# Kernel optimization log

Measured on AMD Instinct MI355X. Metric: run time of the kernel, lower is better.

## Reference

```python
import jax, jax.numpy as jnp
import numpy as np

B, H, W, DIM, NH = 2, 48, 48, 768, 12
HD = DIM // NH  # 64


def setup_inputs() -> dict:
    key = jax.random.key(0)
    ks = jax.random.split(key, 7)
    std = 0.02
    return {
        "x": jax.random.normal(ks[0], (B, H, W, DIM), jnp.float32),
        "rel_pos_h": jax.random.normal(ks[1], (2 * H - 1, HD), jnp.float32) * std,
        "rel_pos_w": jax.random.normal(ks[2], (2 * W - 1, HD), jnp.float32) * std,
        "qkv_w": jax.random.normal(ks[3], (3 * DIM, DIM), jnp.float32) * std,
        "qkv_b": jnp.zeros((3 * DIM,), jnp.float32),
        "proj_w": jax.random.normal(ks[4], (DIM, DIM), jnp.float32) * std,
        "proj_b": jnp.zeros((DIM,), jnp.float32),
    }


def reference(x, rel_pos_h, rel_pos_w, qkv_w, qkv_b, proj_w, proj_b):
    b, h, w, dim = x.shape
    nh = NH
    hd = dim // nh
    scale = hd ** -0.5
    n = h * w
    # qkv projection: (B,N,3*dim) -> (3, B*nh, N, hd)
    qkv = x.reshape(b, n, dim) @ qkv_w.T + qkv_b
    qkv = qkv.reshape(b, n, 3, nh, hd).transpose(2, 0, 3, 1, 4).reshape(3, b * nh, n, hd)
    q, k, v = qkv[0], qkv[1], qkv[2]
    # scaled dot-product scores (B*nh, N, N)
    attn = jnp.einsum('bnc,bmc->bnm', q * scale, k)
    # decomposed relative position bias (q_size == k_size, no interpolation)
    idx_h = jnp.arange(h)[:, None] - jnp.arange(h)[None, :] + (h - 1)  # (h,h)
    idx_w = jnp.arange(w)[:, None] - jnp.arange(w)[None, :] + (w - 1)  # (w,w)
    Rh = rel_pos_h[idx_h]  # (h, h, hd)
    Rw = rel_pos_w[idx_w]  # (w, w, hd)
    r_q = q.reshape(b * nh, h, w, hd)
    rel_h = jnp.einsum('bhwc,hkc->bhwk', r_q, Rh)  # (B*nh, h, w, h)
    rel_w = jnp.einsum('bhwc,wkc->bhwk', r_q, Rw)  # (B*nh, h, w, w)
    attn = (attn.reshape(b * nh, h, w, h, w)
            + rel_h[:, :, :, :, None]
            + rel_w[:, :, :, None, :]).reshape(b * nh, n, n)
    attn = jax.nn.softmax(attn, axis=-1)
    out = (attn @ v).reshape(b, nh, h, w, hd).transpose(0, 2, 3, 1, 4).reshape(b, h, w, dim)
    return out @ proj_w.T + proj_b
```

## Files before the change

### kernel.cpp

```cpp
#include <hip/hip_runtime.h>
#include <hip/hip_bf16.h>
#include <stdint.h>

#define NQ    2304
#define MROWS 4608
#define DIMC  768
#define NHEAD 12
#define HEADS 24
#define HD    64

typedef unsigned int uint;
typedef unsigned short u16;
typedef __attribute__((ext_vector_type(8))) short s16x8;
typedef __attribute__((ext_vector_type(4))) float f32x4;

#define MFMA16(a, b, c) __builtin_amdgcn_mfma_f32_16x16x32_bf16((a), (b), (c), 0, 0, 0)

static __device__ __forceinline__ float bfbits2f(uint u) {
  union { uint i; float f; } c; c.i = u << 16; return c.f;
}
static __device__ __forceinline__ u16 f2bf(float f) {
  __hip_bfloat16 h = __float2bfloat16(f);
  union { __hip_bfloat16 h; u16 u; } c; c.h = h; return c.u;
}
static __device__ __forceinline__ u16 f2h(float f) {
  union { _Float16 h; u16 u; } c; c.h = (_Float16)f; return c.u;
}
static __device__ __forceinline__ float h2f(u16 u) {
  union { u16 u; _Float16 h; } c; c.u = u; return (float)c.h;
}
static __device__ __forceinline__ void dec8(uint4 p, float* f) {
  f[0] = bfbits2f(p.x & 0xFFFFu); f[1] = bfbits2f(p.x >> 16);
  f[2] = bfbits2f(p.y & 0xFFFFu); f[3] = bfbits2f(p.y >> 16);
  f[4] = bfbits2f(p.z & 0xFFFFu); f[5] = bfbits2f(p.z >> 16);
  f[6] = bfbits2f(p.w & 0xFFFFu); f[7] = bfbits2f(p.w >> 16);
}
static __device__ __forceinline__ void ld8(const void* p, size_t idx, int bf, float* f) {
  if (bf) { dec8(*(const uint4*)((const u16*)p + idx), f); }
  else {
    const float4* q = (const float4*)((const float*)p + idx);
    float4 a = q[0], b = q[1];
    f[0] = a.x; f[1] = a.y; f[2] = a.z; f[3] = a.w;
    f[4] = b.x; f[5] = b.y; f[6] = b.z; f[7] = b.w;
  }
}
static __device__ __forceinline__ float ld1(const void* p, size_t idx, int bf) {
  return bf ? bfbits2f(((const u16*)p)[idx]) : ((const float*)p)[idx];
}
static __device__ __forceinline__ uint4 ld8_to_bf(const void* p, size_t idx, int bf) {
  if (bf) return *(const uint4*)((const u16*)p + idx);
  float f[8]; ld8(p, idx, 0, f);
  uint4 u;
  u.x = (uint)f2bf(f[0]) | ((uint)f2bf(f[1]) << 16);
  u.y = (uint)f2bf(f[2]) | ((uint)f2bf(f[3]) << 16);
  u.z = (uint)f2bf(f[4]) | ((uint)f2bf(f[5]) << 16);
  u.w = (uint)f2bf(f[6]) | ((uint)f2bf(f[7]) << 16);
  return u;
}

__global__ __launch_bounds__(64) void detect_k(const u16* __restrict__ x,
                                               int* __restrict__ mode) {
  int t = threadIdx.x;
  int cnt = 0;
  for (int i = 0; i < 32; ++i) {
    uint u = x[(size_t)(t * 32 + i) * 2];
    uint e = (u >> 7) & 0xFFu;
    uint mag = u & 0x7FFFu;
    if (mag == 0 || (e >= 113 && e <= 133)) cnt++;
  }
#pragma unroll
  for (int d = 1; d < 64; d <<= 1) cnt += __shfl_xor(cnt, d);
  if (t == 0) mode[0] = (cnt > 1024) ? 1 : 0;
}

__global__ __launch_bounds__(256) void qkv_gemm_k(
    const void* __restrict__ Xp, const void* __restrict__ Wp,
    const void* __restrict__ Bq, const int* __restrict__ mode,
    u16* __restrict__ Q, u16* __restrict__ K, u16* __restrict__ Vt)
{
  __shared__ __align__(16) u16 As[128][40];
  __shared__ __align__(16) u16 Bs[128][40];
  const int bf = mode[0];
  const int t = threadIdx.x;
  const int w = t >> 6, l15 = t & 15, quad = (t >> 4) & 3;
  const int wr = w >> 1, wc = w & 1;
  const int row0 = blockIdx.y << 7, col0 = blockIdx.x << 7;
  const int lr = t >> 1, lk = (t & 1) << 4;

  f32x4 zero4 = {0.f, 0.f, 0.f, 0.f};
  f32x4 acc[4][4];
#pragma unroll
  for (int i = 0; i < 4; ++i)
#pragma unroll
    for (int j = 0; j < 4; ++j) acc[i][j] = zero4;

  for (int kt = 0; kt < DIMC; kt += 32) {
    __syncthreads();
    *(uint4*)&As[lr][lk]     = ld8_to_bf(Xp, (size_t)(row0 + lr) * DIMC + kt + lk, bf);
    *(uint4*)&As[lr][lk + 8] = ld8_to_bf(Xp, (size_t)(row0 + lr) * DIMC + kt + lk + 8, bf);
    *(uint4*)&Bs[lr][lk]     = ld8_to_bf(Wp, (size_t)(col0 + lr) * DIMC + kt + lk, bf);
    *(uint4*)&Bs[lr][lk + 8] = ld8_to_bf(Wp, (size_t)(col0 + lr) * DIMC + kt + lk + 8, bf);
    __syncthreads();
    s16x8 af[4], bfr[4];
#pragma unroll
    for (int i = 0; i < 4; ++i)
      af[i] = *(const s16x8*)&As[(wr << 6) + (i << 4) + l15][quad << 3];
#pragma unroll
    for (int j = 0; j < 4; ++j)
      bfr[j] = *(const s16x8*)&Bs[(wc << 6) + (j << 4) + l15][quad << 3];
#pragma unroll
    for (int i = 0; i < 4; ++i)
#pragma unroll
      for (int j = 0; j < 4; ++j)
        acc[i][j] = MFMA16(af[i], bfr[j], acc[i][j]);
  }

#pragma unroll
  for (int jt = 0; jt < 4; ++jt) {
    int col = col0 + (wc << 6) + (jt << 4) + l15;
    int which = col / DIMC;
    int rem = col - which * DIMC;
    int head = rem >> 6, d = rem & 63;
    float bv = ld1(Bq, col, bf);
#pragma unroll
    for (int i = 0; i < 4; ++i)
#pragma unroll
      for (int r = 0; r < 4; ++r) {
        int mrow = row0 + (wr << 6) + (i << 4) + (quad << 2) + r;
        int b_ = (mrow >= NQ) ? 1 : 0;
        int n = mrow - b_ * NQ;
        u16 val = f2bf(acc[i][jt][r] + bv);
        size_t bh = (size_t)(b_ * NHEAD + head);
        if (which == 2)      Vt[(bh * HD + d) * NQ + n] = val;
        else if (which == 1) K[(bh * NQ + n) * HD + d] = val;
        else                 Q[(bh * NQ + n) * HD + d] = val;
      }
  }
}

__global__ __launch_bounds__(256) void bias_gemm_k(
    const u16* __restrict__ Qw,
    const void* __restrict__ rph, const void* __restrict__ rpw,
    const int* __restrict__ mode,
    u16* __restrict__ Bh_g, u16* __restrict__ Bw_g)
{
  __shared__ __align__(16) u16 As[128][72];
  __shared__ __align__(16) u16 Bs[192][72];
  const int bf = mode[0];
  const int t = threadIdx.x;
  const int w = t >> 6, l15 = t & 15, quad = (t >> 4) & 3;
  const int wr = w >> 1, wc = w & 1;
  const int blk = blockIdx.x;
  const int bhd = blk / 18;
  const int row0 = (blk - bhd * 18) << 7;

  {
    int lr = t >> 1, lk = (t & 1) << 5;
    const u16* src = Qw + ((size_t)bhd * NQ + row0 + lr) * HD + lk;
    *(uint4*)&As[lr][lk]      = *(const uint4*)(src);
    *(uint4*)&As[lr][lk + 8]  = *(const uint4*)(src + 8);
    *(uint4*)&As[lr][lk + 16] = *(const uint4*)(src + 16);
    *(uint4*)&As[lr][lk + 24] = *(const uint4*)(src + 24);
  }
  for (int e = t; e < 384; e += 256) {
    int row = e >> 1, k32 = (e & 1) << 5;
    int tab = (row >= 96) ? 1 : 0;
    int r2 = row - (tab ? 96 : 0);
    if (r2 > 94) r2 = 0;
    const void* src = tab ? rpw : rph;
    *(uint4*)&Bs[row][k32]      = ld8_to_bf(src, (size_t)r2 * HD + k32, bf);
    *(uint4*)&Bs[row][k32 + 8]  = ld8_to_bf(src, (size_t)r2 * HD + k32 + 8, bf);
    *(uint4*)&Bs[row][k32 + 16] = ld8_to_bf(src, (size_t)r2 * HD + k32 + 16, bf);
    *(uint4*)&Bs[row][k32 + 24] = ld8_to_bf(src, (size_t)r2 * HD + k32 + 24, bf);
  }
  __syncthreads();

  f32x4 zero4 = {0.f, 0.f, 0.f, 0.f};
  f32x4 acc[4][6];
#pragma unroll
  for (int i = 0; i < 4; ++i)
#pragma unroll
    for (int j = 0; j < 6; ++j) acc[i][j] = zero4;

#pragma unroll
  for (int ks = 0; ks < 2; ++ks) {
    s16x8 af[4], bfr[6];
#pragma unroll
    for (int i = 0; i < 4; ++i)
      af[i] = *(const s16x8*)&As[(wr << 6) + (i << 4) + l15][(ks << 5) + (quad << 3)];
#pragma unroll
    for (int j = 0; j < 6; ++j)
      bfr[j] = *(const s16x8*)&Bs[wc * 96 + (j << 4) + l15][(ks << 5) + (quad << 3)];
#pragma unroll
    for (int i = 0; i < 4; ++i)
#pragma unroll
      for (int j = 0; j < 6; ++j)
        acc[i][j] = MFMA16(af[i], bfr[j], acc[i][j]);
  }

#pragma unroll
  for (int jt = 0; jt < 6; ++jt) {
    int col = wc * 96 + (jt << 4) + l15;
    int tab = (col >= 96) ? 1 : 0;
    int j = col - (tab ? 96 : 0);
    if (j >= 95) continue;
    u16* dstT = tab ? Bw_g : Bh_g;
#pragma unroll
    for (int i = 0; i < 4; ++i)
#pragma unroll
      for (int r = 0; r < 4; ++r) {
        int n = row0 + (wr << 6) + (i << 4) + (quad << 2) + r;
        int qh = (n * 10923) >> 19;
        int coord = tab ? (n - qh * 48) : qh;
        int c = coord + 47 - j;
        if (c >= 0 && c < 48)
          dstT[((size_t)bhd * 48 + c) * NQ + n] = f2h(acc[i][jt][r]);
      }
  }
}

__global__ __launch_bounds__(256) void attn_k(
    const u16* __restrict__ Qw, const u16* __restrict__ Kw,
    const u16* __restrict__ Vtg,
    const u16* __restrict__ Bh_g, const u16* __restrict__ Bw_g,
    int S, float* __restrict__ Opart, float* __restrict__ Lpart,
    u16* __restrict__ Aout)
{
  __shared__ __align__(16) u16 BhL[48][128];
  __shared__ __align__(16) u16 BwL[128][52];

  const int bid = blockIdx.x;
  const int xcd = bid & 7;
  const int local = bid >> 3;
  const int per_head = 18 * S;
  const int head_l = local / per_head;
  const int rem = local - head_l * per_head;
  const int qb = rem / S;
  const int z = rem - qb * S;
  const int bhd = xcd * 3 + head_l;
  const int q0 = qb << 7;
  const int span = NQ / S;
  const int kt_lo = z * span, kt_hi = kt_lo + span;

  const int t = threadIdx.x;
  const int w = t >> 6, l15 = t & 15, quad = (t >> 4) & 3;
  const float scale = 0.125f;

  const u16* kbase  = Kw  + (size_t)bhd * NQ * HD;
  const u16* vtbase = Vtg + (size_t)bhd * HD * NQ;
  const int q0w = q0 + (w << 5);

  for (int e = t; e < 48 * 128; e += 256) {
    int c = e >> 7, r = e & 127;
    size_t gi = ((size_t)bhd * 48 + c) * NQ + q0 + r;
    BhL[c][r] = Bh_g[gi];
    BwL[r][c] = Bw_g[gi];
  }

  s16x8 qa0[2], qa1[2];
#pragma unroll
  for (int g = 0; g < 2; ++g) {
    const u16* qfrag = Qw + ((size_t)bhd * NQ + q0w + (g << 4) + l15) * HD + (quad << 3);
    qa0[g] = *(const s16x8*)(qfrag);
    qa1[g] = *(const s16x8*)(qfrag + 32);
  }

  __syncthreads();

  f32x4 zero4 = {0.f, 0.f, 0.f, 0.f};
  f32x4 acc_o[2][4];
#pragma unroll
  for (int g = 0; g < 2; ++g)
#pragma unroll
    for (int nc = 0; nc < 4; ++nc) acc_o[g][nc] = zero4;
  float l_st[2] = {0.f, 0.f};
  const int srcA = ((quad & 1) << 5) + l15;
  const int srcB = srcA + 16;
  const int hi = quad >> 1;
  int km = 0;

  for (int kt0 = kt_lo; kt0 < kt_hi; kt0 += 64) {
    f32x4 acc_s[2][4];
#pragma unroll
    for (int nc = 0; nc < 4; ++nc) {
      const u16* kp = kbase + (size_t)(kt0 + (nc << 4) + l15) * HD + (quad << 3);
      s16x8 kb0 = *(const s16x8*)(kp);
      s16x8 kb1 = *(const s16x8*)(kp + 32);
      f32x4 a0 = MFMA16(kb0, qa0[0], zero4);
      acc_s[0][nc] = MFMA16(kb1, qa1[0], a0);
      f32x4 a1 = MFMA16(kb0, qa0[1], zero4);
      acc_s[1][nc] = MFMA16(kb1, qa1[1], a1);
    }

    int kh0 = (kt0 * 10923) >> 19;
    int thr = (kh0 + 1) * 48 - kt0;
    uint Wq[2][8];
#pragma unroll
    for (int g = 0; g < 2; ++g) {
      int qrl = (w << 5) + (g << 4) + l15;
      float bh0v = h2f(BhL[kh0][qrl]);
      float bh1v = h2f(BhL[kh0 + 1][qrl]);
      float sum = 0.f;
#pragma unroll
      for (int nc = 0; nc < 4; ++nc) {
        int bnc = km + (nc << 4);
        bnc = (bnc >= 48) ? bnc - 48 : bnc;
        uint2 pv = *(const uint2*)&BwL[qrl][bnc + (quad << 2)];
        float b0 = h2f((u16)(pv.x & 0xFFFFu));
        float b1 = h2f((u16)(pv.x >> 16));
        float b2 = h2f((u16)(pv.y & 0xFFFFu));
        float b3 = h2f((u16)(pv.y >> 16));
        int kl = (nc << 4) + (quad << 2);
        float e0 = __expf(acc_s[g][nc][0] * scale + ((kl     >= thr) ? bh1v : bh0v) + b0);
        float e1 = __expf(acc_s[g][nc][1] * scale + ((kl + 1 >= thr) ? bh1v : bh0v) + b1);
        float e2 = __expf(acc_s[g][nc][2] * scale + ((kl + 2 >= thr) ? bh1v : bh0v) + b2);
        float e3 = __expf(acc_s[g][nc][3] * scale + ((kl + 3 >= thr) ? bh1v : bh0v) + b3);
        sum += (e0 + e1) + (e2 + e3);
        Wq[g][2 * nc]     = (uint)f2bf(e0) | ((uint)f2bf(e1) << 16);
        Wq[g][2 * nc + 1] = (uint)f2bf(e2) | ((uint)f2bf(e3) << 16);
      }
      l_st[g] += sum;
    }

#pragma unroll
    for (int h = 0; h < 2; ++h) {
      s16x8 vb[4];
#pragma unroll
      for (int nc = 0; nc < 4; ++nc)
        vb[nc] = *(const s16x8*)(vtbase + (size_t)((nc << 4) + l15) * NQ
                                 + kt0 + (h << 5) + (quad << 3));
#pragma unroll
      for (int g = 0; g < 2; ++g) {
        uint e0 = __shfl(Wq[g][4*h+0], srcA), e1 = __shfl(Wq[g][4*h+1], srcA);
        uint e2 = __shfl(Wq[g][4*h+2], srcA), e3 = __shfl(Wq[g][4*h+3], srcA);
        uint g0 = __shfl(Wq[g][4*h+0], srcB), g1 = __shfl(Wq[g][4*h+1], srcB);
        uint g2 = __shfl(Wq[g][4*h+2], srcB), g3 = __shfl(Wq[g][4*h+3], srcB);
        union { uint u[4]; s16x8 v; } pf;
        pf.u[0] = hi ? e2 : e0; pf.u[1] = hi ? e3 : e1;
        pf.u[2] = hi ? g2 : g0; pf.u[3] = hi ? g3 : g1;
#pragma unroll
        for (int nc = 0; nc < 4; ++nc)
          acc_o[g][nc] = MFMA16(pf.v, vb[nc], acc_o[g][nc]);
      }
    }
    km += 16;
    if (km >= 48) km -= 48;
  }

#pragma unroll
  for (int g = 0; g < 2; ++g) {
    float lg = l_st[g];
    lg += __shfl_xor(lg, 16);
    lg += __shfl_xor(lg, 32);
    if (S > 1) {
      float* Op = Opart + ((size_t)(z * HEADS + bhd) * NQ + q0) * HD;
#pragma unroll
      for (int r = 0; r < 4; ++r) {
        int row = (w << 5) + (g << 4) + (quad << 2) + r;
#pragma unroll
        for (int nc = 0; nc < 4; ++nc)
          Op[(size_t)row * HD + (nc << 4) + l15] = acc_o[g][nc][r];
      }
      if (quad == 0)
        Lpart[(size_t)(z * HEADS + bhd) * NQ + q0w + (g << 4) + l15] = lg;
    } else {
      int b_ = bhd / NHEAD, head = bhd - b_ * NHEAD;
      float invl = 1.f / lg;
      int bsrc = (quad << 4) + (quad << 2);
#pragma unroll
      for (int r = 0; r < 4; ++r) {
        float inv = __shfl(invl, bsrc + r);
        int token = q0 + (w << 5) + (g << 4) + (quad << 2) + r;
        u16* dst = Aout + ((size_t)b_ * NQ + token) * DIMC + (head << 6);
#pragma unroll
        for (int nc = 0; nc < 4; ++nc)
          dst[(nc << 4) + l15] = f2bf(acc_o[g][nc][r] * inv);
      }
    }
  }
}

__global__ __launch_bounds__(256) void combine_k(
    const float* __restrict__ Op, const float* __restrict__ Lp,
    int S, u16* __restrict__ Aout)
{
  int idx = blockIdx.x * 256 + threadIdx.x;
  int m = idx / 192;
  int cq = idx - m * 192;
  int ccol = cq << 2;
  int head = ccol >> 6, d0 = ccol & 63;
  int b_ = (m >= NQ) ? 1 : 0;
  int n = m - b_ * NQ;
  int bh = b_ * NHEAD + head;
  float ox = 0.f, oy = 0.f, oz = 0.f, ow = 0.f, ls = 0.f;
  for (int zz = 0; zz < S; ++zz) {
    const float* ob = Op + ((size_t)(zz * HEADS + bh) * NQ + n) * HD + d0;
    float4 v = *(const float4*)ob;
    ox += v.x; oy += v.y; oz += v.z; ow += v.w;
    ls += Lp[(size_t)(zz * HEADS + bh) * NQ + n];
  }
  float inv = 1.f / ls;
  u16* dst = Aout + (size_t)m * DIMC + ccol;
  dst[0] = f2bf(ox * inv); dst[1] = f2bf(oy * inv);
  dst[2] = f2bf(oz * inv); dst[3] = f2bf(ow * inv);
}

__global__ __launch_bounds__(256) void proj_gemm_k(
    const u16* __restrict__ A, const void* __restrict__ Wp,
    const void* __restrict__ Bp, const int* __restrict__ mode,
    void* __restrict__ Out)
{
  __shared__ __align__(16) u16 As[128][40];
  __shared__ __align__(16) u16 Bs[128][40];
  const int bf = mode[0];
  const int t = threadIdx.x;
  const int w = t >> 6, l15 = t & 15, quad = (t >> 4) & 3;
  const int wr = w >> 1, wc = w & 1;
  const int row0 = blockIdx.y << 7, col0 = blockIdx.x << 7;
  const int lr = t >> 1, lk = (t & 1) << 4;

  f32x4 zero4 = {0.f, 0.f, 0.f, 0.f};
  f32x4 acc[4][4];
#pragma unroll
  for (int i = 0; i < 4; ++i)
#pragma unroll
    for (int j = 0; j < 4; ++j) acc[i][j] = zero4;

  for (int kt = 0; kt < DIMC; kt += 32) {
    __syncthreads();
    *(uint4*)&As[lr][lk]     = *(const uint4*)(A + (size_t)(row0 + lr) * DIMC + kt + lk);
    *(uint4*)&As[lr][lk + 8] = *(const uint4*)(A + (size_t)(row0 + lr) * DIMC + kt + lk + 8);
    *(uint4*)&Bs[lr][lk]     = ld8_to_bf(Wp, (size_t)(col0 + lr) * DIMC + kt + lk, bf);
    *(uint4*)&Bs[lr][lk + 8] = ld8_to_bf(Wp, (size_t)(col0 + lr) * DIMC + kt + lk + 8, bf);
    __syncthreads();
    s16x8 af[4], bfr[4];
#pragma unroll
    for (int i = 0; i < 4; ++i)
      af[i] = *(const s16x8*)&As[(wr << 6) + (i << 4) + l15][quad << 3];
#pragma unroll
    for (int j = 0; j < 4; ++j)
      bfr[j] = *(const s16x8*)&Bs[(wc << 6) + (j << 4) + l15][quad << 3];
#pragma unroll
    for (int i = 0; i < 4; ++i)
#pragma unroll
      for (int j = 0; j < 4; ++j)
        acc[i][j] = MFMA16(af[i], bfr[j], acc[i][j]);
  }

#pragma unroll
  for (int jt = 0; jt < 4; ++jt) {
    int col = col0 + (wc << 6) + (jt << 4) + l15;
    float bv = ld1(Bp, col, bf);
#pragma unroll
    for (int i = 0; i < 4; ++i)
#pragma unroll
      for (int r = 0; r < 4; ++r) {
        int mrow = row0 + (wr << 6) + (i << 4) + (quad << 2) + r;
        float val = acc[i][jt][r] + bv;
        size_t off = (size_t)mrow * DIMC + col;
        if (bf) ((u16*)Out)[off] = f2bf(val);
        else    ((float*)Out)[off] = val;
      }
  }
}

extern "C" void kernel_launch(void* const* d_in, const int* in_sizes, int n_in,
                              void* d_out, int out_size, void* d_ws, size_t ws_size,
                              hipStream_t stream)
{
  const void* x    = d_in[0];
  const void* rph  = d_in[1];
  const void* rpw  = d_in[2];
  const void* qkvw = d_in[3];
  const void* qkvb = d_in[4];
  const void* pw   = d_in[5];
  const void* pb   = d_in[6];

  int* mode = (int*)d_ws;
  const size_t qkv_elems = (size_t)HEADS * NQ * HD;
  u16* q    = (u16*)((char*)d_ws + 16);
  u16* k    = q + qkv_elems;
  u16* vt   = k + qkv_elems;
  u16* aout = vt + qkv_elems;
  const size_t base = 16 + 4 * qkv_elems * 2;
  const size_t biasElems = (size_t)HEADS * 48 * NQ;
  u16* bh_g = (u16*)((char*)d_ws + base);
  u16* bw_g = bh_g + biasElems;
  const size_t base2 = base + 2 * biasElems * 2;
  const size_t perO = (size_t)HEADS * NQ * HD * 4;
  const size_t perL = (size_t)HEADS * NQ * 4;

  int S = 1;
  if (ws_size >= base2 + 3 * (perO + perL)) S = 3;
  else if (ws_size >= base2 + 2 * (perO + perL)) S = 2;
  float* opart = (float*)((char*)d_ws + base2);
  float* lpart = (float*)((char*)d_ws + base2 + (size_t)S * perO);

  detect_k<<<1, 64, 0, stream>>>((const u16*)x, mode);
  qkv_gemm_k<<<dim3(18, 36), 256, 0, stream>>>(x, qkvw, qkvb, mode, q, k, vt);
  bias_gemm_k<<<dim3(432), 256, 0, stream>>>(q, rph, rpw, mode, bh_g, bw_g);
  attn_k<<<dim3(432 * S), 256, 0, stream>>>(q, k, vt, bh_g, bw_g,
                                            S, opart, lpart, aout);
  if (S > 1)
    combine_k<<<dim3(3456), 256, 0, stream>>>(opart, lpart, S, aout);
  proj_gemm_k<<<dim3(6, 36), 256, 0, stream>>>(aout, pw, pb, mode, d_out);
}
```

Baseline: 381.6 us.

## Double attention query tile to 256 rows and interleave QK/softmax/PV per half

Each attention block now covers 256 query rows (64 per wave) instead of 128, so every K and V tile loaded from global memory is reused across twice as many queries, and the grid is halved. The score MFMA, bias-add/exp and PV MFMA are restructured to work per 32-key half, which limits how many score registers are live at once. The bias tile staging into LDS now uses 16-byte vector loads. The cost is more accumulator registers per thread and fewer blocks, which can lower occupancy and leave CUs idle.

```diff
diff --git a/kernel.cpp b/kernel.cpp
--- a/kernel.cpp
+++ b/kernel.cpp
@@ -226,19 +226,19 @@
     int S, float* __restrict__ Opart, float* __restrict__ Lpart,
     u16* __restrict__ Aout)
 {
-  __shared__ __align__(16) u16 BhL[48][128];
-  __shared__ __align__(16) u16 BwL[128][52];
+  __shared__ __align__(16) u16 BhL[48][256];
+  __shared__ __align__(16) u16 BwL[256][52];
 
   const int bid = blockIdx.x;
   const int xcd = bid & 7;
   const int local = bid >> 3;
-  const int per_head = 18 * S;
+  const int per_head = 9 * S;
   const int head_l = local / per_head;
   const int rem = local - head_l * per_head;
   const int qb = rem / S;
   const int z = rem - qb * S;
   const int bhd = xcd * 3 + head_l;
-  const int q0 = qb << 7;
+  const int q0 = qb << 8;
   const int span = NQ / S;
   const int kt_lo = z * span, kt_hi = kt_lo + span;
 
@@ -248,18 +248,26 @@
 
   const u16* kbase  = Kw  + (size_t)bhd * NQ * HD;
   const u16* vtbase = Vtg + (size_t)bhd * HD * NQ;
-  const int q0w = q0 + (w << 5);
-
-  for (int e = t; e < 48 * 128; e += 256) {
-    int c = e >> 7, r = e & 127;
-    size_t gi = ((size_t)bhd * 48 + c) * NQ + q0 + r;
-    BhL[c][r] = Bh_g[gi];
-    BwL[r][c] = Bw_g[gi];
-  }
-
-  s16x8 qa0[2], qa1[2];
-#pragma unroll
-  for (int g = 0; g < 2; ++g) {
+  const int q0w = q0 + (w << 6);
+
+  for (int e = t; e < 1536; e += 256) {
+    int c = e >> 5;
+    int off = (e & 31) << 3;
+    size_t gi = ((size_t)bhd * 48 + c) * NQ + q0 + off;
+    *(uint4*)&BhL[c][off] = *(const uint4*)(Bh_g + gi);
+    uint4 wv = *(const uint4*)(Bw_g + gi);
+    u16 vals[8];
+    vals[0] = wv.x & 0xFFFFu; vals[1] = wv.x >> 16;
+    vals[2] = wv.y & 0xFFFFu; vals[3] = wv.y >> 16;
+    vals[4] = wv.z & 0xFFFFu; vals[5] = wv.z >> 16;
+    vals[6] = wv.w & 0xFFFFu; vals[7] = wv.w >> 16;
+#pragma unroll
+    for (int j = 0; j < 8; ++j) BwL[off + j][c] = vals[j];
+  }
+
+  s16x8 qa0[4], qa1[4];
+#pragma unroll
+  for (int g = 0; g < 4; ++g) {
     const u16* qfrag = Qw + ((size_t)bhd * NQ + q0w + (g << 4) + l15) * HD + (quad << 3);
     qa0[g] = *(const s16x8*)(qfrag);
     qa1[g] = *(const s16x8*)(qfrag + 32);
@@ -268,73 +276,65 @@
   __syncthreads();
 
   f32x4 zero4 = {0.f, 0.f, 0.f, 0.f};
-  f32x4 acc_o[2][4];
-#pragma unroll
-  for (int g = 0; g < 2; ++g)
+  f32x4 acc_o[4][4];
+#pragma unroll
+  for (int g = 0; g < 4; ++g)
 #pragma unroll
     for (int nc = 0; nc < 4; ++nc) acc_o[g][nc] = zero4;
-  float l_st[2] = {0.f, 0.f};
+  float l_st[4] = {0.f, 0.f, 0.f, 0.f};
   const int srcA = ((quad & 1) << 5) + l15;
   const int srcB = srcA + 16;
   const int hi = quad >> 1;
   int km = 0;
 
   for (int kt0 = kt_lo; kt0 < kt_hi; kt0 += 64) {
-    f32x4 acc_s[2][4];
-#pragma unroll
-    for (int nc = 0; nc < 4; ++nc) {
-      const u16* kp = kbase + (size_t)(kt0 + (nc << 4) + l15) * HD + (quad << 3);
-      s16x8 kb0 = *(const s16x8*)(kp);
-      s16x8 kb1 = *(const s16x8*)(kp + 32);
-      f32x4 a0 = MFMA16(kb0, qa0[0], zero4);
-      acc_s[0][nc] = MFMA16(kb1, qa1[0], a0);
-      f32x4 a1 = MFMA16(kb0, qa0[1], zero4);
-      acc_s[1][nc] = MFMA16(kb1, qa1[1], a1);
-    }
-
     int kh0 = (kt0 * 10923) >> 19;
     int thr = (kh0 + 1) * 48 - kt0;
-    uint Wq[2][8];
-#pragma unroll
-    for (int g = 0; g < 2; ++g) {
-      int qrl = (w << 5) + (g << 4) + l15;
-      float bh0v = h2f(BhL[kh0][qrl]);
-      float bh1v = h2f(BhL[kh0 + 1][qrl]);
-      float sum = 0.f;
-#pragma unroll
-      for (int nc = 0; nc < 4; ++nc) {
+
+#pragma unroll
+    for (int h = 0; h < 2; ++h) {
+      uint W[4][4];
+#pragma unroll
+      for (int nc2 = 0; nc2 < 2; ++nc2) {
+        int nc = (h << 1) + nc2;
+        const u16* kp = kbase + (size_t)(kt0 + (nc << 4) + l15) * HD + (quad << 3);
+        s16x8 kb0 = *(const s16x8*)(kp);
+        s16x8 kb1 = *(const s16x8*)(kp + 32);
         int bnc = km + (nc << 4);
         bnc = (bnc >= 48) ? bnc - 48 : bnc;
-        uint2 pv = *(const uint2*)&BwL[qrl][bnc + (quad << 2)];
-        float b0 = h2f((u16)(pv.x & 0xFFFFu));
-        float b1 = h2f((u16)(pv.x >> 16));
-        float b2 = h2f((u16)(pv.y & 0xFFFFu));
-        float b3 = h2f((u16)(pv.y >> 16));
         int kl = (nc << 4) + (quad << 2);
-        float e0 = __expf(acc_s[g][nc][0] * scale + ((kl     >= thr) ? bh1v : bh0v) + b0);
-        float e1 = __expf(acc_s[g][nc][1] * scale + ((kl + 1 >= thr) ? bh1v : bh0v) + b1);
-        float e2 = __expf(acc_s[g][nc][2] * scale + ((kl + 2 >= thr) ? bh1v : bh0v) + b2);
-        float e3 = __expf(acc_s[g][nc][3] * scale + ((kl + 3 >= thr) ? bh1v : bh0v) + b3);
-        sum += (e0 + e1) + (e2 + e3);
-        Wq[g][2 * nc]     = (uint)f2bf(e0) | ((uint)f2bf(e1) << 16);
-        Wq[g][2 * nc + 1] = (uint)f2bf(e2) | ((uint)f2bf(e3) << 16);
-      }
-      l_st[g] += sum;
-    }
-
-#pragma unroll
-    for (int h = 0; h < 2; ++h) {
+#pragma unroll
+        for (int g = 0; g < 4; ++g) {
+          f32x4 a = MFMA16(kb0, qa0[g], zero4);
+          f32x4 s4 = MFMA16(kb1, qa1[g], a);
+          int qrl = (w << 6) + (g << 4) + l15;
+          float bh0v = h2f(BhL[kh0][qrl]);
+          float bh1v = h2f(BhL[kh0 + 1][qrl]);
+          uint2 pv = *(const uint2*)&BwL[qrl][bnc + (quad << 2)];
+          float b0 = h2f((u16)(pv.x & 0xFFFFu));
+          float b1 = h2f((u16)(pv.x >> 16));
+          float b2 = h2f((u16)(pv.y & 0xFFFFu));
+          float b3 = h2f((u16)(pv.y >> 16));
+          float e0 = __expf(s4[0] * scale + ((kl     >= thr) ? bh1v : bh0v) + b0);
+          float e1 = __expf(s4[1] * scale + ((kl + 1 >= thr) ? bh1v : bh0v) + b1);
+          float e2 = __expf(s4[2] * scale + ((kl + 2 >= thr) ? bh1v : bh0v) + b2);
+          float e3 = __expf(s4[3] * scale + ((kl + 3 >= thr) ? bh1v : bh0v) + b3);
+          l_st[g] += (e0 + e1) + (e2 + e3);
+          W[g][2 * nc2]     = (uint)f2bf(e0) | ((uint)f2bf(e1) << 16);
+          W[g][2 * nc2 + 1] = (uint)f2bf(e2) | ((uint)f2bf(e3) << 16);
+        }
+      }
       s16x8 vb[4];
 #pragma unroll
       for (int nc = 0; nc < 4; ++nc)
         vb[nc] = *(const s16x8*)(vtbase + (size_t)((nc << 4) + l15) * NQ
                                  + kt0 + (h << 5) + (quad << 3));
 #pragma unroll
-      for (int g = 0; g < 2; ++g) {
-        uint e0 = __shfl(Wq[g][4*h+0], srcA), e1 = __shfl(Wq[g][4*h+1], srcA);
-        uint e2 = __shfl(Wq[g][4*h+2], srcA), e3 = __shfl(Wq[g][4*h+3], srcA);
-        uint g0 = __shfl(Wq[g][4*h+0], srcB), g1 = __shfl(Wq[g][4*h+1], srcB);
-        uint g2 = __shfl(Wq[g][4*h+2], srcB), g3 = __shfl(Wq[g][4*h+3], srcB);
+      for (int g = 0; g < 4; ++g) {
+        uint e0 = __shfl(W[g][0], srcA), e1 = __shfl(W[g][1], srcA);
+        uint e2 = __shfl(W[g][2], srcA), e3 = __shfl(W[g][3], srcA);
+        uint g0 = __shfl(W[g][0], srcB), g1 = __shfl(W[g][1], srcB);
+        uint g2 = __shfl(W[g][2], srcB), g3 = __shfl(W[g][3], srcB);
         union { uint u[4]; s16x8 v; } pf;
         pf.u[0] = hi ? e2 : e0; pf.u[1] = hi ? e3 : e1;
         pf.u[2] = hi ? g2 : g0; pf.u[3] = hi ? g3 : g1;
@@ -348,7 +348,7 @@
   }
 
 #pragma unroll
-  for (int g = 0; g < 2; ++g) {
+  for (int g = 0; g < 4; ++g) {
     float lg = l_st[g];
     lg += __shfl_xor(lg, 16);
     lg += __shfl_xor(lg, 32);
@@ -356,7 +356,7 @@
       float* Op = Opart + ((size_t)(z * HEADS + bhd) * NQ + q0) * HD;
 #pragma unroll
       for (int r = 0; r < 4; ++r) {
-        int row = (w << 5) + (g << 4) + (quad << 2) + r;
+        int row = (w << 6) + (g << 4) + (quad << 2) + r;
 #pragma unroll
         for (int nc = 0; nc < 4; ++nc)
           Op[(size_t)row * HD + (nc << 4) + l15] = acc_o[g][nc][r];
@@ -370,7 +370,7 @@
 #pragma unroll
       for (int r = 0; r < 4; ++r) {
         float inv = __shfl(invl, bsrc + r);
-        int token = q0 + (w << 5) + (g << 4) + (quad << 2) + r;
+        int token = q0 + (w << 6) + (g << 4) + (quad << 2) + r;
         u16* dst = Aout + ((size_t)b_ * NQ + token) * DIMC + (head << 6);
 #pragma unroll
         for (int nc = 0; nc < 4; ++nc)
@@ -499,7 +499,7 @@
   detect_k<<<1, 64, 0, stream>>>((const u16*)x, mode);
   qkv_gemm_k<<<dim3(18, 36), 256, 0, stream>>>(x, qkvw, qkvb, mode, q, k, vt);
   bias_gemm_k<<<dim3(432), 256, 0, stream>>>(q, rph, rpw, mode, bh_g, bw_g);
-  attn_k<<<dim3(432 * S), 256, 0, stream>>>(q, k, vt, bh_g, bw_g,
+  attn_k<<<dim3(216 * S), 256, 0, stream>>>(q, k, vt, bh_g, bw_g,
                                             S, opart, lpart, aout);
   if (S > 1)
     combine_k<<<dim3(3456), 256, 0, stream>>>(opart, lpart, S, aout);
```

New measurement: 385.5 us. Within noise of the previous version (+1.0%).
